# Kernel optimization log

Measured on AMD Instinct MI355X. Metric: run time of the kernel, lower is better.

## Reference

```python
import jax, jax.numpy as jnp
import numpy as np

D_IN = 1024
D_OUT = 1024
NUM_HEADS = 16
D_HEAD = D_OUT // NUM_HEADS


def setup_inputs() -> dict:
    key = jax.random.key(0)
    ks = jax.random.split(key, 6)
    s = 0.02
    return {
        "x": jax.random.normal(ks[0], (2, 2048, D_IN), dtype=jnp.float32),
        "W_q": jax.random.normal(ks[1], (D_IN, D_OUT), dtype=jnp.float32) * s,
        "W_k": jax.random.normal(ks[2], (D_IN, D_OUT), dtype=jnp.float32) * s,
        "W_v": jax.random.normal(ks[3], (D_IN, D_OUT), dtype=jnp.float32) * s,
        "W_o": jax.random.normal(ks[4], (D_OUT, D_OUT), dtype=jnp.float32) * s,
        "b_o": jax.random.normal(ks[5], (D_OUT,), dtype=jnp.float32) * s,
    }


def reference(x, W_q, W_k, W_v, W_o, b_o):
    B, T, _ = x.shape
    # qkv projections (no bias), split heads -> [B, H, T, d_head]
    def split_heads(t):
        return t.reshape(B, T, NUM_HEADS, D_HEAD).transpose(0, 2, 1, 3)
    q = split_heads(x @ W_q)
    k = split_heads(x @ W_k)
    v = split_heads(x @ W_v)
    # full causal scores [B, H, T, T]
    scores = jnp.einsum("bhqd,bhkd->bhqk", q, k)
    causal = jnp.triu(jnp.ones((T, T), dtype=bool), k=1)
    scores = jnp.where(causal, -jnp.inf, scores)
    attn = jax.nn.softmax(scores / np.sqrt(D_HEAD).astype(np.float32), axis=-1)
    # dropout rate is 0.0 -> identity
    ctx = jnp.einsum("bhqk,bhkd->bhqd", attn, v)
    ctx = ctx.transpose(0, 2, 1, 3).reshape(B, T, D_OUT)
    return ctx @ W_o + b_o
```

## Files before the change

### kernel.cpp

```cpp
#include <hip/hip_runtime.h>
#include <hip/hip_bf16.h>
#include <cstdint>

#define SEQ_T 2048
#define DMODEL 1024
#define NHEAD 16
#define DHEAD 64

typedef __attribute__((ext_vector_type(8))) __bf16 bf16x8;
typedef __attribute__((ext_vector_type(4))) float floatx4;

static __device__ __forceinline__ uint16_t f2bf(float f) {
    union { float f; uint32_t u; } v; v.f = f;
    uint32_t r = v.u + 0x7FFFu + ((v.u >> 16) & 1u);
    return (uint16_t)(r >> 16);
}

__global__ void mha_cvt_x(const float* __restrict__ x, uint16_t* __restrict__ xb) {
    int i = (blockIdx.x * blockDim.x + threadIdx.x) * 4;
    float4 f = *(const float4*)(x + i);
    union { uint16_t u[4]; uint64_t v; } o;
    o.u[0] = f2bf(f.x); o.u[1] = f2bf(f.y); o.u[2] = f2bf(f.z); o.u[3] = f2bf(f.w);
    *(uint64_t*)(xb + i) = o.v;
}

__global__ void mha_cvt_wt(const float* __restrict__ W0, const float* __restrict__ W1,
                           const float* __restrict__ W2, const float* __restrict__ W3,
                           uint16_t* __restrict__ T0, uint16_t* __restrict__ T1,
                           uint16_t* __restrict__ T2, uint16_t* __restrict__ T3) {
    const float* W; uint16_t* Tt;
    switch (blockIdx.z) {
        case 0: W = W0; Tt = T0; break;
        case 1: W = W1; Tt = T1; break;
        case 2: W = W2; Tt = T2; break;
        default: W = W3; Tt = T3; break;
    }
    __shared__ float tile[64][65];
    const int c  = threadIdx.x & 63;
    const int r0 = threadIdx.x >> 6;
    const int R0 = blockIdx.y * 64, C0 = blockIdx.x * 64;
#pragma unroll
    for (int rr = 0; rr < 16; ++rr) {
        int r = r0 + rr * 4;
        tile[r][c] = W[(size_t)(R0 + r) * DMODEL + C0 + c];
    }
    __syncthreads();
#pragma unroll
    for (int rr = 0; rr < 16; ++rr) {
        int r = r0 + rr * 4;
        Tt[(size_t)(C0 + r) * DMODEL + R0 + c] = f2bf(tile[c][r]);
    }
}

template<int MODE>
__device__ __forceinline__ void gemm128_body(
    const uint16_t* __restrict__ A, const uint16_t* __restrict__ Bt,
    uint16_t* __restrict__ outB, float* __restrict__ outF,
    const float* __restrict__ bias) {
    const int K = DMODEL, N = DMODEL;
    __shared__ uint16_t As[2][128 * 32];
    __shared__ uint16_t Bs[2][128 * 32];
    const int tid  = threadIdx.x;
    const int wave = tid >> 6;
    const int lane = tid & 63;
    const int m0 = blockIdx.y * 128;
    const int n0 = blockIdx.x * 128;
    const int lr   = lane & 15;
    const int quad = lane >> 4;
    const int wm = wave >> 1, wn = wave & 1;

    floatx4 acc[4][4];
#pragma unroll
    for (int i = 0; i < 4; ++i)
#pragma unroll
        for (int j = 0; j < 4; ++j) acc[i][j] = (floatx4)0.0f;

    auto stage = [&](int k0, int buf) {
#pragma unroll
        for (int i = 0; i < 2; ++i) {
            int chunk = i * 256 + wave * 64 + lane;
            int r  = chunk >> 2;
            int c8 = (chunk & 3) * 8;
            const uint16_t* ga = A  + (size_t)(m0 + r) * K + k0 + c8;
            const uint16_t* gb = Bt + (size_t)(n0 + r) * K + k0 + c8;
            uint16_t* la = &As[buf][(size_t)(i * 256 + wave * 64) * 8];
            uint16_t* lb = &Bs[buf][(size_t)(i * 256 + wave * 64) * 8];
            __builtin_amdgcn_global_load_lds((const __attribute__((address_space(1))) void*)ga,
                                             (__attribute__((address_space(3))) void*)la, 16, 0, 0);
            __builtin_amdgcn_global_load_lds((const __attribute__((address_space(1))) void*)gb,
                                             (__attribute__((address_space(3))) void*)lb, 16, 0, 0);
        }
    };

    stage(0, 0);
    __syncthreads();
    int cur = 0;
    for (int k0 = 0; k0 < K; k0 += 32) {
        if (k0 + 32 < K) stage(k0 + 32, cur ^ 1);
        bf16x8 af[4], bfr[4];
#pragma unroll
        for (int mi = 0; mi < 4; ++mi)
            af[mi] = *(const bf16x8*)&As[cur][(wm * 64 + mi * 16 + lr) * 32 + quad * 8];
#pragma unroll
        for (int ni = 0; ni < 4; ++ni)
            bfr[ni] = *(const bf16x8*)&Bs[cur][(wn * 64 + ni * 16 + lr) * 32 + quad * 8];
#pragma unroll
        for (int mi = 0; mi < 4; ++mi)
#pragma unroll
            for (int ni = 0; ni < 4; ++ni)
                acc[mi][ni] = __builtin_amdgcn_mfma_f32_16x16x32_bf16(af[mi], bfr[ni], acc[mi][ni], 0, 0, 0);
        __syncthreads();
        cur ^= 1;
    }
#pragma unroll
    for (int mi = 0; mi < 4; ++mi)
#pragma unroll
        for (int ni = 0; ni < 4; ++ni) {
            int col = n0 + wn * 64 + ni * 16 + lr;
            if (MODE == 1) {
                int row0 = m0 + wm * 64 + mi * 16 + quad * 4;
                union { uint16_t u[4]; uint64_t v8; } pk;
#pragma unroll
                for (int r = 0; r < 4; ++r) pk.u[r] = f2bf(acc[mi][ni][r]);
                int bb = row0 >> 11, t = row0 & 2047;
                *(uint64_t*)&outB[((size_t)(bb * 1024 + col)) * 2048 + t] = pk.v8;
            } else {
#pragma unroll
                for (int r = 0; r < 4; ++r) {
                    int row = m0 + wm * 64 + mi * 16 + quad * 4 + r;
                    float v = acc[mi][ni][r];
                    if (MODE == 2) outF[(size_t)row * N + col] = v + bias[col];
                    else           outB[(size_t)row * N + col] = f2bf(v);
                }
            }
        }
}

__global__ __launch_bounds__(256) void mha_gemm_qkv(
    const uint16_t* __restrict__ A,
    const uint16_t* __restrict__ Wq, const uint16_t* __restrict__ Wk, const uint16_t* __restrict__ Wv,
    uint16_t* __restrict__ Q, uint16_t* __restrict__ K, uint16_t* __restrict__ Vt) {
    switch (blockIdx.z) {
        case 0:  gemm128_body<0>(A, Wq, Q,  nullptr, nullptr); break;
        case 1:  gemm128_body<0>(A, Wk, K,  nullptr, nullptr); break;
        default: gemm128_body<1>(A, Wv, Vt, nullptr, nullptr); break;
    }
}

__global__ __launch_bounds__(256) void mha_gemm_out(
    const uint16_t* __restrict__ A, const uint16_t* __restrict__ Wot,
    float* __restrict__ out, const float* __restrict__ bias) {
    gemm128_body<2>(A, Wot, nullptr, out, bias);
}

__global__ __launch_bounds__(256) void mha_attn_mfma(
    const uint16_t* __restrict__ Q, const uint16_t* __restrict__ K,
    const uint16_t* __restrict__ Vt, uint16_t* __restrict__ ctx) {
    __shared__ alignas(16) uint16_t Ks[2][64 * 64];
    __shared__ alignas(16) uint16_t Vs[2][64 * 64];
    __shared__ alignas(16) uint16_t Pb[64 * 72];

    const int tid  = threadIdx.x;
    const int wave = tid >> 6;
    const int lane = tid & 63;
    const int lr   = lane & 15;
    const int quad = lane >> 4;
    const int p  = blockIdx.x;
    const int h  = blockIdx.y;
    const int b  = blockIdx.z;
    const int jH = 31 - p, jL = p;
    const int TH = jH + 1;
    const int TL = jL + 1;
    const int Ttot = TH + TL;

    int wrow = jH * 64 + wave * 16;
    bf16x8 qf0, qf1;
    {
        const size_t qb = ((size_t)(b * SEQ_T) + wrow + lr) * DMODEL + h * DHEAD;
        qf0 = *(const bf16x8*)(Q + qb + quad * 8);
        qf1 = *(const bf16x8*)(Q + qb + 32 + quad * 8);
    }
    floatx4 o[4];
#pragma unroll
    for (int nt = 0; nt < 4; ++nt) o[nt] = (floatx4)0.0f;
    float l[4] = {0.f, 0.f, 0.f, 0.f};

    auto stage = [&](int kv0, int buf) {
#pragma unroll
        for (int i = 0; i < 2; ++i) {
            int c = i * 256 + tid;
            int row = c >> 3, cs = c & 7;
            int csk = cs ^ (row & 7);
            const uint16_t* gk = K  + ((size_t)(b * SEQ_T) + kv0 + row) * DMODEL + h * DHEAD + csk * 8;
            const uint16_t* gv = Vt + ((size_t)(b * 1024 + h * DHEAD + row)) * 2048 + kv0 + csk * 8;
            uint16_t* lk = &Ks[buf][(i * 256 + wave * 64) * 8];
            uint16_t* lv = &Vs[buf][(i * 256 + wave * 64) * 8];
            __builtin_amdgcn_global_load_lds((const __attribute__((address_space(1))) void*)gk,
                                             (__attribute__((address_space(3))) void*)lk, 16, 0, 0);
            __builtin_amdgcn_global_load_lds((const __attribute__((address_space(1))) void*)gv,
                                             (__attribute__((address_space(3))) void*)lv, 16, 0, 0);
        }
    };
    auto epilogue = [&]() {
#pragma unroll
        for (int r = 0; r < 4; ++r) {
            float v = l[r];
            v += __shfl_xor(v, 1, 64);
            v += __shfl_xor(v, 2, 64);
            v += __shfl_xor(v, 4, 64);
            v += __shfl_xor(v, 8, 64);
            l[r] = 1.f / v;
        }
#pragma unroll
        for (int nt = 0; nt < 4; ++nt)
#pragma unroll
            for (int r = 0; r < 4; ++r) {
                size_t addr = ((size_t)(b * SEQ_T) + wrow + quad * 4 + r) * DMODEL + h * DHEAD + nt * 16 + lr;
                ctx[addr] = f2bf(o[nt][r] * l[r]);
            }
    };

    stage(0, 0);
    __syncthreads();
    int cur = 0;

    for (int t = 0; t < Ttot; ++t) {
        if (t + 1 < Ttot) {
            int nkv0 = ((t + 1 < TH) ? (t + 1) : (t + 1 - TH)) * 64;
            stage(nkv0, cur ^ 1);
        }
        const int kv0 = ((t < TH) ? t : (t - TH)) * 64;

        floatx4 s[4];
#pragma unroll
        for (int nt = 0; nt < 4; ++nt) {
            s[nt] = (floatx4)0.0f;
            int krow = nt * 16 + lr;
#pragma unroll
            for (int ks = 0; ks < 2; ++ks) {
                bf16x8 kf = *(const bf16x8*)&Ks[cur][krow * 64 + (((ks * 4 + quad) ^ (lr & 7)) * 8)];
                s[nt] = __builtin_amdgcn_mfma_f32_16x16x32_bf16(ks ? qf1 : qf0, kf, s[nt], 0, 0, 0);
            }
        }
        if (kv0 + 63 > wrow) {
#pragma unroll
            for (int nt = 0; nt < 4; ++nt) {
                int kcol = kv0 + nt * 16 + lr;
#pragma unroll
                for (int r = 0; r < 4; ++r) {
                    int qrow = wrow + quad * 4 + r;
                    if (kcol > qrow) s[nt][r] = -3e38f;
                }
            }
        }
#pragma unroll
        for (int nt = 0; nt < 4; ++nt)
#pragma unroll
            for (int r = 0; r < 4; ++r) {
                float pe = __expf(s[nt][r] * 0.125f);
                uint32_t pu = __float_as_uint(pe);
                l[r] += __uint_as_float(pu & 0xffff0000u);
                Pb[(wave * 16 + quad * 4 + r) * 72 + nt * 16 + lr] = (uint16_t)(pu >> 16);
            }
#pragma unroll
        for (int ks = 0; ks < 2; ++ks) {
            bf16x8 pfr = *(const bf16x8*)&Pb[(wave * 16 + lr) * 72 + ks * 32 + quad * 8];
#pragma unroll
            for (int nt = 0; nt < 4; ++nt) {
                int vrow = nt * 16 + lr;
                bf16x8 vf = *(const bf16x8*)&Vs[cur][vrow * 64 + (((ks * 4 + quad) ^ (lr & 7)) * 8)];
                o[nt] = __builtin_amdgcn_mfma_f32_16x16x32_bf16(pfr, vf, o[nt], 0, 0, 0);
            }
        }
        if (t == TH - 1) {
            epilogue();
            wrow = jL * 64 + wave * 16;
            const size_t qb = ((size_t)(b * SEQ_T) + wrow + lr) * DMODEL + h * DHEAD;
            qf0 = *(const bf16x8*)(Q + qb + quad * 8);
            qf1 = *(const bf16x8*)(Q + qb + 32 + quad * 8);
#pragma unroll
            for (int nt = 0; nt < 4; ++nt) o[nt] = (floatx4)0.0f;
#pragma unroll
            for (int r = 0; r < 4; ++r) l[r] = 0.f;
        }
        __syncthreads();
        cur ^= 1;
    }
    epilogue();
}

extern "C" void kernel_launch(void* const* d_in, const int* in_sizes, int n_in,
                              void* d_out, int out_size, void* d_ws, size_t ws_size,
                              hipStream_t stream) {
    const float* x  = (const float*)d_in[0];
    const float* Wq = (const float*)d_in[1];
    const float* Wk = (const float*)d_in[2];
    const float* Wv = (const float*)d_in[3];
    const float* Wo = (const float*)d_in[4];
    const float* bo = (const float*)d_in[5];
    float* out = (float*)d_out;

    char* ws = (char*)d_ws;
    const size_t SZ_X = (size_t)4096 * DMODEL * 2;
    const size_t SZ_W = (size_t)DMODEL * DMODEL * 2;
    size_t off = 0;
    uint16_t* xb  = (uint16_t*)(ws + off); off += SZ_X;
    uint16_t* wqt = (uint16_t*)(ws + off); off += SZ_W;
    uint16_t* wkt = (uint16_t*)(ws + off); off += SZ_W;
    uint16_t* wvt = (uint16_t*)(ws + off); off += SZ_W;
    uint16_t* wot = (uint16_t*)(ws + off); off += SZ_W;
    uint16_t* Qb  = (uint16_t*)(ws + off); off += SZ_X;
    uint16_t* Kb  = (uint16_t*)(ws + off); off += SZ_X;
    uint16_t* Vtb = (uint16_t*)(ws + off); off += SZ_X;
    uint16_t* Cb  = (uint16_t*)(ws + off); off += SZ_X;
    (void)ws_size; (void)in_sizes; (void)n_in; (void)out_size;

    mha_cvt_x<<<4096, 256, 0, stream>>>(x, xb);
    mha_cvt_wt<<<dim3(16, 16, 4), 256, 0, stream>>>(Wq, Wk, Wv, Wo, wqt, wkt, wvt, wot);
    mha_gemm_qkv<<<dim3(8, 32, 3), 256, 0, stream>>>(xb, wqt, wkt, wvt, Qb, Kb, Vtb);
    mha_attn_mfma<<<dim3(16, NHEAD, 2), 256, 0, stream>>>(Qb, Kb, Vtb, Cb);
    mha_gemm_out<<<dim3(8, 32, 1), 256, 0, stream>>>(Cb, wot, out, bo);
}
```

Measured before the change: 197.1 us.

## Single-buffer GEMM LDS, stage V transpose via LDS, split out-proj into 128x64 tiles

Removes double buffering from the shared GEMM body, so each k-step loads, syncs, computes and syncs, with half the LDS. The transposed V output is staged through an LDS tile so rows are written to global memory with wide coalesced stores. The output projection becomes its own kernel with 128x64 tiles and twice as many blocks, to fill more CUs. The attention kernel hoists its K/V address computation out of the staging lambda. Dropping the double buffer gives up load/compute overlap in exchange for lower LDS use and higher occupancy.

```diff
diff --git a/kernel.cpp b/kernel.cpp
--- a/kernel.cpp
+++ b/kernel.cpp
@@ -55,11 +55,10 @@
 template<int MODE>
 __device__ __forceinline__ void gemm128_body(
     const uint16_t* __restrict__ A, const uint16_t* __restrict__ Bt,
-    uint16_t* __restrict__ outB, float* __restrict__ outF,
-    const float* __restrict__ bias) {
+    uint16_t* __restrict__ outB) {
     const int K = DMODEL, N = DMODEL;
-    __shared__ uint16_t As[2][128 * 32];
-    __shared__ uint16_t Bs[2][128 * 32];
+    __shared__ uint16_t As[128 * 32];
+    __shared__ uint16_t Bs[128 * 32];
     const int tid  = threadIdx.x;
     const int wave = tid >> 6;
     const int lane = tid & 63;
@@ -75,7 +74,7 @@
 #pragma unroll
         for (int j = 0; j < 4; ++j) acc[i][j] = (floatx4)0.0f;
 
-    auto stage = [&](int k0, int buf) {
+    for (int k0 = 0; k0 < K; k0 += 32) {
 #pragma unroll
         for (int i = 0; i < 2; ++i) {
             int chunk = i * 256 + wave * 64 + lane;
@@ -83,57 +82,71 @@
             int c8 = (chunk & 3) * 8;
             const uint16_t* ga = A  + (size_t)(m0 + r) * K + k0 + c8;
             const uint16_t* gb = Bt + (size_t)(n0 + r) * K + k0 + c8;
-            uint16_t* la = &As[buf][(size_t)(i * 256 + wave * 64) * 8];
-            uint16_t* lb = &Bs[buf][(size_t)(i * 256 + wave * 64) * 8];
+            uint16_t* la = &As[(size_t)(i * 256 + wave * 64) * 8];
+            uint16_t* lb = &Bs[(size_t)(i * 256 + wave * 64) * 8];
             __builtin_amdgcn_global_load_lds((const __attribute__((address_space(1))) void*)ga,
                                              (__attribute__((address_space(3))) void*)la, 16, 0, 0);
             __builtin_amdgcn_global_load_lds((const __attribute__((address_space(1))) void*)gb,
                                              (__attribute__((address_space(3))) void*)lb, 16, 0, 0);
         }
-    };
-
-    stage(0, 0);
-    __syncthreads();
-    int cur = 0;
-    for (int k0 = 0; k0 < K; k0 += 32) {
-        if (k0 + 32 < K) stage(k0 + 32, cur ^ 1);
+        __syncthreads();
         bf16x8 af[4], bfr[4];
 #pragma unroll
         for (int mi = 0; mi < 4; ++mi)
-            af[mi] = *(const bf16x8*)&As[cur][(wm * 64 + mi * 16 + lr) * 32 + quad * 8];
+            af[mi] = *(const bf16x8*)&As[(wm * 64 + mi * 16 + lr) * 32 + quad * 8];
 #pragma unroll
         for (int ni = 0; ni < 4; ++ni)
-            bfr[ni] = *(const bf16x8*)&Bs[cur][(wn * 64 + ni * 16 + lr) * 32 + quad * 8];
+            bfr[ni] = *(const bf16x8*)&Bs[(wn * 64 + ni * 16 + lr) * 32 + quad * 8];
 #pragma unroll
         for (int mi = 0; mi < 4; ++mi)
 #pragma unroll
             for (int ni = 0; ni < 4; ++ni)
                 acc[mi][ni] = __builtin_amdgcn_mfma_f32_16x16x32_bf16(af[mi], bfr[ni], acc[mi][ni], 0, 0, 0);
         __syncthreads();
-        cur ^= 1;
-    }
-#pragma unroll
-    for (int mi = 0; mi < 4; ++mi)
-#pragma unroll
-        for (int ni = 0; ni < 4; ++ni) {
-            int col = n0 + wn * 64 + ni * 16 + lr;
-            if (MODE == 1) {
-                int row0 = m0 + wm * 64 + mi * 16 + quad * 4;
-                union { uint16_t u[4]; uint64_t v8; } pk;
-#pragma unroll
-                for (int r = 0; r < 4; ++r) pk.u[r] = f2bf(acc[mi][ni][r]);
-                int bb = row0 >> 11, t = row0 & 2047;
-                *(uint64_t*)&outB[((size_t)(bb * 1024 + col)) * 2048 + t] = pk.v8;
-            } else {
+    }
+    if constexpr (MODE == 1) {
+        __shared__ uint16_t Ct[64][136];
+        const int bb = m0 >> 11;
+        const int t0 = m0 & 2047;
+#pragma unroll
+        for (int p = 0; p < 2; ++p) {
+            if (wn == p) {
+#pragma unroll
+                for (int mi = 0; mi < 4; ++mi)
+#pragma unroll
+                    for (int ni = 0; ni < 4; ++ni) {
+                        int cl = ni * 16 + lr;
+                        int tl = wm * 64 + mi * 16 + quad * 4;
+                        union { uint16_t u[4]; uint64_t v8; } pk;
+#pragma unroll
+                        for (int r = 0; r < 4; ++r) pk.u[r] = f2bf(acc[mi][ni][r]);
+                        *(uint64_t*)&Ct[cl][tl] = pk.v8;
+                    }
+            }
+            __syncthreads();
+#pragma unroll
+            for (int k = 0; k < 4; ++k) {
+                int c  = k * 256 + tid;
+                int cl = c >> 4;
+                int off = (c & 15) * 8;
+                uint4 v = *(const uint4*)&Ct[cl][off];
+                *(uint4*)&outB[((size_t)(bb * 1024 + n0 + p * 64 + cl)) * 2048 + t0 + off] = v;
+            }
+            __syncthreads();
+        }
+    } else {
+#pragma unroll
+        for (int mi = 0; mi < 4; ++mi)
+#pragma unroll
+            for (int ni = 0; ni < 4; ++ni) {
+                int col = n0 + wn * 64 + ni * 16 + lr;
 #pragma unroll
                 for (int r = 0; r < 4; ++r) {
                     int row = m0 + wm * 64 + mi * 16 + quad * 4 + r;
-                    float v = acc[mi][ni][r];
-                    if (MODE == 2) outF[(size_t)row * N + col] = v + bias[col];
-                    else           outB[(size_t)row * N + col] = f2bf(v);
+                    outB[(size_t)row * N + col] = f2bf(acc[mi][ni][r]);
                 }
             }
-        }
+    }
 }
 
 __global__ __launch_bounds__(256) void mha_gemm_qkv(
@@ -141,16 +154,80 @@
     const uint16_t* __restrict__ Wq, const uint16_t* __restrict__ Wk, const uint16_t* __restrict__ Wv,
     uint16_t* __restrict__ Q, uint16_t* __restrict__ K, uint16_t* __restrict__ Vt) {
     switch (blockIdx.z) {
-        case 0:  gemm128_body<0>(A, Wq, Q,  nullptr, nullptr); break;
-        case 1:  gemm128_body<0>(A, Wk, K,  nullptr, nullptr); break;
-        default: gemm128_body<1>(A, Wv, Vt, nullptr, nullptr); break;
+        case 0:  gemm128_body<0>(A, Wq, Q);  break;
+        case 1:  gemm128_body<0>(A, Wk, K);  break;
+        default: gemm128_body<1>(A, Wv, Vt); break;
     }
 }
 
 __global__ __launch_bounds__(256) void mha_gemm_out(
     const uint16_t* __restrict__ A, const uint16_t* __restrict__ Wot,
     float* __restrict__ out, const float* __restrict__ bias) {
-    gemm128_body<2>(A, Wot, nullptr, out, bias);
+    const int K = DMODEL, N = DMODEL;
+    __shared__ uint16_t As[128 * 32];
+    __shared__ uint16_t Bs[64 * 32];
+    const int tid  = threadIdx.x;
+    const int wave = tid >> 6;
+    const int lane = tid & 63;
+    const int m0 = blockIdx.y * 128;
+    const int n0 = blockIdx.x * 64;
+    const int lr   = lane & 15;
+    const int quad = lane >> 4;
+    const int wm = wave >> 1, wn = wave & 1;
+
+    floatx4 acc[4][2];
+#pragma unroll
+    for (int i = 0; i < 4; ++i)
+#pragma unroll
+        for (int j = 0; j < 2; ++j) acc[i][j] = (floatx4)0.0f;
+
+    for (int k0 = 0; k0 < K; k0 += 32) {
+#pragma unroll
+        for (int i = 0; i < 2; ++i) {
+            int chunk = i * 256 + wave * 64 + lane;
+            int r  = chunk >> 2;
+            int c8 = (chunk & 3) * 8;
+            const uint16_t* ga = A + (size_t)(m0 + r) * K + k0 + c8;
+            uint16_t* la = &As[(size_t)(i * 256 + wave * 64) * 8];
+            __builtin_amdgcn_global_load_lds((const __attribute__((address_space(1))) void*)ga,
+                                             (__attribute__((address_space(3))) void*)la, 16, 0, 0);
+        }
+        {
+            int chunk = wave * 64 + lane;
+            int r  = chunk >> 2;
+            int c8 = (chunk & 3) * 8;
+            const uint16_t* gb = Wot + (size_t)(n0 + r) * K + k0 + c8;
+            uint16_t* lb = &Bs[(size_t)(wave * 64) * 8];
+            __builtin_amdgcn_global_load_lds((const __attribute__((address_space(1))) void*)gb,
+                                             (__attribute__((address_space(3))) void*)lb, 16, 0, 0);
+        }
+        __syncthreads();
+        bf16x8 af[4], bfr[2];
+#pragma unroll
+        for (int mi = 0; mi < 4; ++mi)
+            af[mi] = *(const bf16x8*)&As[(wm * 64 + mi * 16 + lr) * 32 + quad * 8];
+#pragma unroll
+        for (int ni = 0; ni < 2; ++ni)
+            bfr[ni] = *(const bf16x8*)&Bs[(wn * 32 + ni * 16 + lr) * 32 + quad * 8];
+#pragma unroll
+        for (int mi = 0; mi < 4; ++mi)
+#pragma unroll
+            for (int ni = 0; ni < 2; ++ni)
+                acc[mi][ni] = __builtin_amdgcn_mfma_f32_16x16x32_bf16(af[mi], bfr[ni], acc[mi][ni], 0, 0, 0);
+        __syncthreads();
+    }
+#pragma unroll
+    for (int mi = 0; mi < 4; ++mi)
+#pragma unroll
+        for (int ni = 0; ni < 2; ++ni) {
+            int col = n0 + wn * 32 + ni * 16 + lr;
+            float bv = bias[col];
+#pragma unroll
+            for (int r = 0; r < 4; ++r) {
+                int row = m0 + wm * 64 + mi * 16 + quad * 4 + r;
+                out[(size_t)row * N + col] = acc[mi][ni][r] + bv;
+            }
+        }
 }
 
 __global__ __launch_bounds__(256) void mha_attn_mfma(
@@ -173,6 +250,17 @@
     const int TL = jL + 1;
     const int Ttot = TH + TL;
 
+    const uint16_t* kbase[2];
+    const uint16_t* vbase[2];
+#pragma unroll
+    for (int i = 0; i < 2; ++i) {
+        int c = i * 256 + tid;
+        int row = c >> 3, cs = c & 7;
+        int csk = cs ^ (row & 7);
+        kbase[i] = K  + ((size_t)(b * SEQ_T) + row) * DMODEL + h * DHEAD + csk * 8;
+        vbase[i] = Vt + ((size_t)(b * 1024 + h * DHEAD + row)) * 2048 + csk * 8;
+    }
+
     int wrow = jH * 64 + wave * 16;
     bf16x8 qf0, qf1;
     {
@@ -188,11 +276,8 @@
     auto stage = [&](int kv0, int buf) {
 #pragma unroll
         for (int i = 0; i < 2; ++i) {
-            int c = i * 256 + tid;
-            int row = c >> 3, cs = c & 7;
-            int csk = cs ^ (row & 7);
-            const uint16_t* gk = K  + ((size_t)(b * SEQ_T) + kv0 + row) * DMODEL + h * DHEAD + csk * 8;
-            const uint16_t* gv = Vt + ((size_t)(b * 1024 + h * DHEAD + row)) * 2048 + kv0 + csk * 8;
+            const uint16_t* gk = kbase[i] + (size_t)kv0 * DMODEL;
+            const uint16_t* gv = vbase[i] + kv0;
             uint16_t* lk = &Ks[buf][(i * 256 + wave * 64) * 8];
             uint16_t* lv = &Vs[buf][(i * 256 + wave * 64) * 8];
             __builtin_amdgcn_global_load_lds((const __attribute__((address_space(1))) void*)gk,
@@ -319,5 +404,5 @@
     mha_cvt_wt<<<dim3(16, 16, 4), 256, 0, stream>>>(Wq, Wk, Wv, Wo, wqt, wkt, wvt, wot);
     mha_gemm_qkv<<<dim3(8, 32, 3), 256, 0, stream>>>(xb, wqt, wkt, wvt, Qb, Kb, Vtb);
     mha_attn_mfma<<<dim3(16, NHEAD, 2), 256, 0, stream>>>(Qb, Kb, Vtb, Cb);
-    mha_gemm_out<<<dim3(8, 32, 1), 256, 0, stream>>>(Cb, wot, out, bo);
-}
+    mha_gemm_out<<<dim3(16, 32), 256, 0, stream>>>(Cb, wot, out, bo);
+}
```

New measurement: 201.6 us. +2.3%, slower.
